# Kernel optimization log

Hardware: AMD Instinct MI355X
Metric: run time of the kernel (lower is better)

## Reference

```python
import jax, jax.numpy as jnp
import numpy as np

KERNEL_SIZE = 7
K2 = KERNEL_SIZE * KERNEL_SIZE


def setup_inputs() -> dict:
    key = jax.random.key(0)
    k1, k2, k3 = jax.random.split(key, 3)
    B, C, H, W = 4, 3, 256, 256
    image = jax.random.normal(k1, (B, C, H, W), dtype=jnp.float32)
    offsets = jax.random.normal(k2, (B, 2 * K2, H, W), dtype=jnp.float32)
    weights = jax.random.uniform(k3, (B, K2, H, W), dtype=jnp.float32)
    return {"image": image, "offsets": offsets, "weights": weights}


def _adacof(image, offsets, weights):
    b, c, h, w = image.shape
    k2 = weights.shape[1]
    # offsets are interleaved (dx_i, dy_i) pairs along channel dim
    off = offsets.reshape(b, k2, 2, h, w)
    dx = off[:, :, 0]  # (B,K2,H,W)
    dy = off[:, :, 1]

    gx = jnp.arange(w, dtype=image.dtype)
    gy = jnp.arange(h, dtype=image.dtype)
    sample_x = gx[None, None, None, :] + dx  # (B,K2,H,W)
    sample_y = gy[None, None, :, None] + dy

    # Faithful to the torch code: coords normalized with the align_corners=True
    # formula (2*s/(size-1)-1) but F.grid_sample called with align_corners=False,
    # whose unnormalization is p = ((g+1)*size - 1)/2.  Composition:
    #   p = s * size/(size-1) - 0.5
    px = sample_x * (w / (w - 1.0)) - 0.5
    py = sample_y * (h / (h - 1.0)) - 0.5

    # padding_mode='border': clip coordinates to valid range before bilinear
    px = jnp.clip(px, 0.0, w - 1.0)
    py = jnp.clip(py, 0.0, h - 1.0)

    x0 = jnp.floor(px)
    y0 = jnp.floor(py)
    wx = px - x0  # (B,K2,H,W)
    wy = py - y0
    x0i = jnp.clip(x0.astype(jnp.int32), 0, w - 1)
    y0i = jnp.clip(y0.astype(jnp.int32), 0, h - 1)
    x1i = jnp.clip(x0i + 1, 0, w - 1)
    y1i = jnp.clip(y0i + 1, 0, h - 1)

    flat = image.reshape(b, c, h * w)

    def gather(yi, xi):
        idx = (yi * w + xi).reshape(b, 1, k2 * h * w)
        return jnp.take_along_axis(flat, idx, axis=2).reshape(b, c, k2, h, w)

    v00 = gather(y0i, x0i)
    v01 = gather(y0i, x1i)
    v10 = gather(y1i, x0i)
    v11 = gather(y1i, x1i)

    wxe = wx[:, None]  # (B,1,K2,H,W)
    wye = wy[:, None]
    bil = (v00 * (1 - wxe) * (1 - wye)
           + v01 * wxe * (1 - wye)
           + v10 * (1 - wxe) * wye
           + v11 * wxe * wye)  # (B,C,K2,H,W)

    # weighted sum over the K^2 taps
    return jnp.einsum('bkhw,bckhw->bchw', weights, bil)


def reference(image, offsets, weights):
    return _adacof(image, offsets, weights)
```

## Files before the change

kernel.cpp:

```cpp
#include <hip/hip_runtime.h>


#define BB 4
#define CC 3
#define HH 256
#define WW 256
#define K2 49
#define HWSZ (HH * WW)
#define SCALE (256.0f / 255.0f)

#define ROWS 21
#define COLS 81
#define NCELL (ROWS * COLS)

__global__ void __launch_bounds__(512)
adacof_tile(const float* __restrict__ img,
            const float* __restrict__ offsets,
            const float* __restrict__ weights,
            float* __restrict__ out) {
    __shared__ float tile[CC][NCELL];
    __shared__ float redbuf[CC][256];

    const int t = threadIdx.x;
    const int h = t >> 8;
    const int pix = t & 255;
    const int tx = pix & 63;
    const int ty = pix >> 6;

    const int bid = blockIdx.x;
    const int b = bid >> 8;
    const int tIdx = bid & 255;
    const int X0 = (tIdx & 3) << 6;
    const int Y0 = (tIdx >> 2) << 2;
    const int OX = X0 - 8, OY = Y0 - 8;

    const float* imgB = img + (size_t)b * (CC * HWSZ);

    #pragma unroll
    for (int c = 0; c < CC; ++c) {
        const float* p = imgB + (size_t)c * HWSZ;
        for (int i = t; i < NCELL; i += 512) {
            int ry = i / COLS;
            int rx = i - ry * COLS;
            int gy = min(max(OY + ry, 0), HH - 1);
            int gx = min(max(OX + rx, 0), WW - 1);
            tile[c][i] = p[gy * WW + gx];
        }
    }
    __syncthreads();

    const int hw = (Y0 + ty) * WW + X0 + tx;
    const int kbase = h * 24;
    const float* offH = offsets + (size_t)b * (2 * K2 * HWSZ)
                                + (size_t)(2 * kbase) * HWSZ + hw;
    const float* wgtH = weights + (size_t)b * (K2 * HWSZ)
                                + (size_t)kbase * HWSZ + hw;

    const float Axt = (float)(X0 + tx) * SCALE - 0.5f - (float)OX;
    const float Ayt = (float)(Y0 + ty) * SCALE - 0.5f - (float)OY;
    const float loX = (float)(-OX), hiX = (float)(WW - 1 - OX);
    const float loY = (float)(-OY), hiY = (float)(HH - 1 - OY);

    float acc0 = 0.0f, acc1 = 0.0f, acc2 = 0.0f;
    int badm = 0;

    const float* t0 = &tile[0][0];
    auto TAP = [&](float dx, float dy, float wg) {
        float f1x = fminf(fmaxf(fmaf(dx, SCALE, Axt), loX), hiX);
        float f1y = fminf(fmaxf(fmaf(dy, SCALE, Ayt), loY), hiY);
        float f2x = fminf(fmaxf(f1x, 0.0f), 79.0f);
        float f2y = fminf(fmaxf(f1y, 0.0f), 19.0f);
        badm |= (f1x != f2x);
        badm |= (f1y != f2y);
        float x0f = floorf(f2x), y0f = floorf(f2y);
        float wx = f2x - x0f, wy = f2y - y0f;
        int i00 = (int)y0f * COLS + (int)x0f;
        float a11 = wx * wy;
        float a10 = wy - a11;
        float a01 = wx - a11;
        float a00 = (1.0f - wx) - a10;
        a00 *= wg; a01 *= wg; a10 *= wg; a11 *= wg;
        float v00 = t0[i00], v01 = t0[i00 + 1];
        float v10 = t0[i00 + COLS], v11 = t0[i00 + COLS + 1];
        acc0 = fmaf(v00, a00, fmaf(v01, a01, fmaf(v10, a10, fmaf(v11, a11, acc0))));
        v00 = t0[NCELL + i00]; v01 = t0[NCELL + i00 + 1];
        v10 = t0[NCELL + i00 + COLS]; v11 = t0[NCELL + i00 + COLS + 1];
        acc1 = fmaf(v00, a00, fmaf(v01, a01, fmaf(v10, a10, fmaf(v11, a11, acc1))));
        v00 = t0[2 * NCELL + i00]; v01 = t0[2 * NCELL + i00 + 1];
        v10 = t0[2 * NCELL + i00 + COLS]; v11 = t0[2 * NCELL + i00 + COLS + 1];
        acc2 = fmaf(v00, a00, fmaf(v01, a01, fmaf(v10, a10, fmaf(v11, a11, acc2))));
    };

    float dxv[2][4], dyv[2][4], wgv[2][4];
    #pragma unroll
    for (int j = 0; j < 4; ++j) {
        dxv[0][j] = offH[(size_t)(2 * j) * HWSZ];
        dyv[0][j] = offH[(size_t)(2 * j + 1) * HWSZ];
        wgv[0][j] = wgtH[(size_t)j * HWSZ];
    }
    float dxt = 0.0f, dyt = 0.0f, wgt = 0.0f;
    if (h == 1) {
        dxt = offH[(size_t)48 * HWSZ];
        dyt = offH[(size_t)49 * HWSZ];
        wgt = wgtH[(size_t)24 * HWSZ];
    }
    __builtin_amdgcn_sched_barrier(0);

    #pragma unroll
    for (int g = 0; g < 6; ++g) {
        if (g < 5) {
            #pragma unroll
            for (int j = 0; j < 4; ++j) {
                int k = 4 * (g + 1) + j;
                dxv[(g + 1) & 1][j] = offH[(size_t)(2 * k) * HWSZ];
                dyv[(g + 1) & 1][j] = offH[(size_t)(2 * k + 1) * HWSZ];
                wgv[(g + 1) & 1][j] = wgtH[(size_t)k * HWSZ];
            }
        }
        __builtin_amdgcn_sched_barrier(0);
        #pragma unroll
        for (int j = 0; j < 4; ++j)
            TAP(dxv[g & 1][j], dyv[g & 1][j], wgv[g & 1][j]);
    }
    if (h == 1) TAP(dxt, dyt, wgt);

    if (__any(badm)) {
        if (badm) {
            const float Axi = (float)(X0 + tx) * SCALE - 0.5f;
            const float Ayi = (float)(Y0 + ty) * SCALE - 0.5f;
            float a0 = 0.0f, a1 = 0.0f, a2 = 0.0f;
            int ntap = (h == 1) ? 25 : 24;
            for (int idx = 0; idx < ntap; ++idx) {
                int k = (idx == 24) ? 48 : (kbase + idx);
                float dx = offsets[(size_t)b * (2 * K2 * HWSZ) + (size_t)(2 * k) * HWSZ + hw];
                float dy = offsets[(size_t)b * (2 * K2 * HWSZ) + (size_t)(2 * k + 1) * HWSZ + hw];
                float wg = weights[(size_t)b * (K2 * HWSZ) + (size_t)k * HWSZ + hw];
                float px = fminf(fmaxf(fmaf(dx, SCALE, Axi), 0.0f), 255.0f);
                float py = fminf(fmaxf(fmaf(dy, SCALE, Ayi), 0.0f), 255.0f);
                float x0f = floorf(px), y0f = floorf(py);
                float wx = px - x0f, wy = py - y0f;
                int ix0 = (int)x0f, iy0 = (int)y0f;
                int ix1 = min(ix0 + 1, WW - 1), iy1 = min(iy0 + 1, HH - 1);
                float w11 = wx * wy, w10 = wy - w11, w01 = wx - w11;
                float w00 = (1.0f - wx) - w10;
                #pragma unroll
                for (int c = 0; c < CC; ++c) {
                    const float* p = imgB + (size_t)c * HWSZ;
                    float bil = p[iy0 * WW + ix0] * w00 + p[iy0 * WW + ix1] * w01
                              + p[iy1 * WW + ix0] * w10 + p[iy1 * WW + ix1] * w11;
                    if (c == 0) a0 = fmaf(wg, bil, a0);
                    else if (c == 1) a1 = fmaf(wg, bil, a1);
                    else a2 = fmaf(wg, bil, a2);
                }
            }
            acc0 = a0; acc1 = a1; acc2 = a2;
        }
    }

    if (h == 1) {
        redbuf[0][pix] = acc0;
        redbuf[1][pix] = acc1;
        redbuf[2][pix] = acc2;
    }
    __syncthreads();
    if (h == 0) {
        acc0 += redbuf[0][pix];
        acc1 += redbuf[1][pix];
        acc2 += redbuf[2][pix];
        float* o = out + (size_t)b * (CC * HWSZ) + hw;
        o[0] = acc0;
        o[HWSZ] = acc1;
        o[2 * HWSZ] = acc2;
    }
}

extern "C" void kernel_launch(void* const* d_in, const int* in_sizes, int n_in,
                              void* d_out, int out_size, void* d_ws, size_t ws_size,
                              hipStream_t stream) {
    const float* image = (const float*)d_in[0];
    const float* offsets = (const float*)d_in[1];
    const float* weights = (const float*)d_in[2];
    float* out = (float*)d_out;

    adacof_tile<<<BB * 256, 512, 0, stream>>>(image, offsets, weights, out);
}
```

Before: 39.46 us.

## Interleave channels 0/1 in shared tile and simplify out-of-tile detection

Stores channels 0 and 1 of the shared image tile as interleaved float2 so each bilinear corner needs one 64-bit LDS read plus one scalar read instead of three scalar reads. It also replaces the two-stage clamp-and-compare fallback detection with a simple |dx|>7 or |dy|>7 test. The aim is fewer LDS instructions and fewer ALU ops per tap. The new test flags more pixels than before, so near image borders more wavefronts may take the slow global-memory fallback. Results should still match, because flagged pixels are recomputed exactly, and an offset within 7 pixels stays inside the 8-pixel halo.

```diff
diff --git a/kernel.cpp b/kernel.cpp
--- a/kernel.cpp
+++ b/kernel.cpp
@@ -18,8 +18,9 @@
             const float* __restrict__ offsets,
             const float* __restrict__ weights,
             float* __restrict__ out) {
-    __shared__ float tile[CC][NCELL];
-    __shared__ float redbuf[CC][256];
+    __shared__ float2 t01[NCELL];
+    __shared__ float  t2[NCELL];
+    __shared__ float  redbuf[CC][256];
 
     const int t = threadIdx.x;
     const int h = t >> 8;
@@ -36,15 +37,18 @@
 
     const float* imgB = img + (size_t)b * (CC * HWSZ);
 
-    #pragma unroll
-    for (int c = 0; c < CC; ++c) {
-        const float* p = imgB + (size_t)c * HWSZ;
+    {
+        const float* p0 = imgB;
+        const float* p1 = imgB + HWSZ;
+        const float* p2 = imgB + 2 * HWSZ;
         for (int i = t; i < NCELL; i += 512) {
             int ry = i / COLS;
             int rx = i - ry * COLS;
             int gy = min(max(OY + ry, 0), HH - 1);
             int gx = min(max(OX + rx, 0), WW - 1);
-            tile[c][i] = p[gy * WW + gx];
+            int gi = gy * WW + gx;
+            t01[i] = make_float2(p0[gi], p1[gi]);
+            t2[i] = p2[gi];
         }
     }
     __syncthreads();
@@ -58,37 +62,35 @@
 
     const float Axt = (float)(X0 + tx) * SCALE - 0.5f - (float)OX;
     const float Ayt = (float)(Y0 + ty) * SCALE - 0.5f - (float)OY;
-    const float loX = (float)(-OX), hiX = (float)(WW - 1 - OX);
-    const float loY = (float)(-OY), hiY = (float)(HH - 1 - OY);
 
     float acc0 = 0.0f, acc1 = 0.0f, acc2 = 0.0f;
     int badm = 0;
 
-    const float* t0 = &tile[0][0];
     auto TAP = [&](float dx, float dy, float wg) {
-        float f1x = fminf(fmaxf(fmaf(dx, SCALE, Axt), loX), hiX);
-        float f1y = fminf(fmaxf(fmaf(dy, SCALE, Ayt), loY), hiY);
-        float f2x = fminf(fmaxf(f1x, 0.0f), 79.0f);
-        float f2y = fminf(fmaxf(f1y, 0.0f), 19.0f);
-        badm |= (f1x != f2x);
-        badm |= (f1y != f2y);
-        float x0f = floorf(f2x), y0f = floorf(f2y);
-        float wx = f2x - x0f, wy = f2y - y0f;
+        badm |= (fabsf(dx) > 7.0f) | (fabsf(dy) > 7.0f);
+        float px = fmaf(dx, SCALE, Axt);
+        float py = fmaf(dy, SCALE, Ayt);
+        px = fminf(fmaxf(px, 0.0f), 79.0f);
+        py = fminf(fmaxf(py, 0.0f), 19.0f);
+        float x0f = floorf(px), y0f = floorf(py);
+        float wx = px - x0f, wy = py - y0f;
         int i00 = (int)y0f * COLS + (int)x0f;
         float a11 = wx * wy;
         float a10 = wy - a11;
         float a01 = wx - a11;
         float a00 = (1.0f - wx) - a10;
         a00 *= wg; a01 *= wg; a10 *= wg; a11 *= wg;
-        float v00 = t0[i00], v01 = t0[i00 + 1];
-        float v10 = t0[i00 + COLS], v11 = t0[i00 + COLS + 1];
-        acc0 = fmaf(v00, a00, fmaf(v01, a01, fmaf(v10, a10, fmaf(v11, a11, acc0))));
-        v00 = t0[NCELL + i00]; v01 = t0[NCELL + i00 + 1];
-        v10 = t0[NCELL + i00 + COLS]; v11 = t0[NCELL + i00 + COLS + 1];
-        acc1 = fmaf(v00, a00, fmaf(v01, a01, fmaf(v10, a10, fmaf(v11, a11, acc1))));
-        v00 = t0[2 * NCELL + i00]; v01 = t0[2 * NCELL + i00 + 1];
-        v10 = t0[2 * NCELL + i00 + COLS]; v11 = t0[2 * NCELL + i00 + COLS + 1];
-        acc2 = fmaf(v00, a00, fmaf(v01, a01, fmaf(v10, a10, fmaf(v11, a11, acc2))));
+        float2 c00 = t01[i00];
+        float2 c01 = t01[i00 + 1];
+        float2 c10 = t01[i00 + COLS];
+        float2 c11 = t01[i00 + COLS + 1];
+        float d00 = t2[i00];
+        float d01 = t2[i00 + 1];
+        float d10 = t2[i00 + COLS];
+        float d11 = t2[i00 + COLS + 1];
+        acc0 = fmaf(c00.x, a00, fmaf(c01.x, a01, fmaf(c10.x, a10, fmaf(c11.x, a11, acc0))));
+        acc1 = fmaf(c00.y, a00, fmaf(c01.y, a01, fmaf(c10.y, a10, fmaf(c11.y, a11, acc1))));
+        acc2 = fmaf(d00, a00, fmaf(d01, a01, fmaf(d10, a10, fmaf(d11, a11, acc2))));
     };
 
     float dxv[2][4], dyv[2][4], wgv[2][4];
```

Result: faster. 35.77 us (-9.4%).
